# Performance work log

Hardware: AMD Instinct MI355X
Metric: run time of the kernel (lower is better)

Reference implementation:

```python
import jax, jax.numpy as jnp
import numpy as np

DEPTH = 10
WIDTH = 128
DIM = 2
N = 1_048_576


def setup_inputs() -> dict:
    key = jax.random.key(0)
    ks = jax.random.split(key, 14)
    x = jax.random.normal(ks[0], (N, DIM), jnp.float32)

    # Orthogonal init for the invertible 1x1 convs (QR of a random matrix),
    # matching Invertible1x1Conv.__init__.
    rng = np.random.default_rng(0)
    conv_w = np.stack([np.linalg.qr(rng.standard_normal((DIM, DIM)))[0]
                       for _ in range(DEPTH)]).astype(np.float32)

    def nrm(k, shape, sc=0.1):
        return sc * jax.random.normal(k, shape, jnp.float32)

    return dict(
        x=x,
        an_scale=jnp.exp(nrm(ks[1], (DEPTH, DIM))),          # outer actnorm, positive
        an_bias=nrm(ks[2], (DEPTH, DIM)),
        conv_w=jnp.asarray(conv_w),                           # [D, 2, 2]
        fc1_w=nrm(ks[3], (DEPTH, WIDTH, DIM // 2), 1.0),      # Linear(1, 128)
        fc1_b=nrm(ks[4], (DEPTH, WIDTH)),
        an1_scale=jnp.exp(nrm(ks[5], (DEPTH, WIDTH))),
        an1_bias=nrm(ks[6], (DEPTH, WIDTH)),
        fc2_w=nrm(ks[7], (DEPTH, WIDTH, WIDTH)),              # Linear(128, 128)
        fc2_b=nrm(ks[8], (DEPTH, WIDTH)),
        an2_scale=jnp.exp(nrm(ks[9], (DEPTH, WIDTH))),
        an2_bias=nrm(ks[10], (DEPTH, WIDTH)),
        fc3_w=nrm(ks[11], (DEPTH, DIM, WIDTH)),               # Linear(128, 2)
        fc3_b=nrm(ks[12], (DEPTH, DIM)),
        log_scale_factor=nrm(ks[13], (DEPTH, DIM)),
    )


def reference(x, an_scale, an_bias, conv_w, fc1_w, fc1_b, an1_scale, an1_bias,
              fc2_w, fc2_b, an2_scale, an2_bias, fc3_w, fc3_b, log_scale_factor):
    z = x
    logdet = jnp.zeros((x.shape[0],), x.dtype)
    half = DIM // 2
    for i in range(DEPTH):  # fixed depth=10, structurally distinct params
        # --- Actnorm ---
        z = (z - an_bias[i]) / an_scale[i]
        logdet = logdet - jnp.sum(jnp.log(jnp.abs(an_scale[i])))
        # --- Invertible 1x1 conv ---
        logdet = logdet + jnp.linalg.slogdet(conv_w[i])[1]
        z = z @ conv_w[i].T
        # --- Affine coupling (inner actnorms are already initialized) ---
        z_a, z_b = z[:, :half], z[:, half:]
        h = jax.nn.relu((z_b @ fc1_w[i].T + fc1_b[i] - an1_bias[i]) / an1_scale[i])
        h = jax.nn.relu((h @ fc2_w[i].T + fc2_b[i] - an2_bias[i]) / an2_scale[i])
        h = (h @ fc3_w[i].T + fc3_b[i]) * jnp.exp(log_scale_factor[i])  # [N, 2]
        t = h[:, 0::2]                         # [N, 1]
        s = jax.nn.sigmoid(h[:, 1::2] + 2.0)   # [N, 1]
        z = jnp.concatenate([s * z_a + t, z_b], axis=1)
        logdet = logdet + jnp.sum(jnp.log(s), axis=1)
    return z, logdet
```

## Files before the change

### kernel.cpp

```cpp
#include <hip/hip_runtime.h>
#include <math.h>


constexpr int kDepth = 10;
constexpr int kWidth = 128;
constexpr float kVMin = -24.0f;
constexpr float kVMax =  24.0f;

__global__ void prep_kernel(
    const float* __restrict__ an_scale, const float* __restrict__ an_bias,
    const float* __restrict__ conv_w,
    const float* __restrict__ fc1_w, const float* __restrict__ fc1_b,
    const float* __restrict__ an1_scale, const float* __restrict__ an1_bias,
    const float* __restrict__ fc2_w, const float* __restrict__ fc2_b,
    const float* __restrict__ an2_scale, const float* __restrict__ an2_bias,
    const float* __restrict__ fc3_b, const float* __restrict__ lsf,
    float* __restrict__ meta, float* __restrict__ kv,
    float* __restrict__ CG, float* __restrict__ CB)
{
  __shared__ float sWT[128 * 129];
  __shared__ float sVs[128], sG[128], sB[128];
  __shared__ float sGs[128], sBs[128];
  __shared__ int   sOrd[128];

  const int l = blockIdx.x;
  const int t = threadIdx.x;

  const float* wl = fc2_w + (size_t)l * kWidth * kWidth;
#pragma unroll 8
  for (int fi = t; fi < 128 * 128; fi += 256) {
    const int k = fi >> 7, j = fi & 127;
    sWT[j * 129 + k] = wl[fi];
  }

  if (t < 128) {
    const float s1 = an1_scale[l*kWidth + t];
    const float g = fc1_w[l*kWidth + t] / s1;
    const float b = (fc1_b[l*kWidth + t] - an1_bias[l*kWidth + t]) / s1;
    float vs, sg;
    if (g > 0.0f)      { vs = -b / g; sg =  1.0f; }
    else if (g < 0.0f) { vs = -b / g; sg = -1.0f; }
    else               { vs = (b > 0.0f) ? -1e30f : 1e30f; sg = (b > 0.0f) ? 1.0f : 0.0f; }
    sG[t] = g; sB[t] = b; sVs[t] = vs;
    sGs[t] = sg * g; sBs[t] = sg * b;
  }
  __syncthreads();

  if (t < 128) {
    const float my = sVs[t];
    int r = 0;
    const float4* vs4 = (const float4*)sVs;
#pragma unroll
    for (int i4 = 0; i4 < 32; ++i4) {
      float4 o = vs4[i4];
      const int ib = i4 * 4;
      r += (o.x < my) || (o.x == my && ib + 0 < t);
      r += (o.y < my) || (o.y == my && ib + 1 < t);
      r += (o.z < my) || (o.z == my && ib + 2 < t);
      r += (o.w < my) || (o.w == my && ib + 3 < t);
    }
    sOrd[r] = t;
  }
  __syncthreads();

  if (t < 128) {
    kv[l*128 + t] = sVs[sOrd[t]];

    float cg = 0.0f;
    float cb = fc2_b[l*kWidth + t] - an2_bias[l*kWidth + t];
    const float4* g4 = (const float4*)sG;
    const float4* b4 = (const float4*)sB;
#pragma unroll
    for (int j4 = 0; j4 < 32; ++j4) {
      float4 G = g4[j4], B = b4[j4];
      const int j = j4 * 4;
      float w0 = sWT[(j + 0) * 129 + t];
      float w1 = sWT[(j + 1) * 129 + t];
      float w2 = sWT[(j + 2) * 129 + t];
      float w3 = sWT[(j + 3) * 129 + t];
      if (G.x < 0.0f) { cg = fmaf(G.x, w0, cg); cb = fmaf(B.x, w0, cb); }
      if (G.y < 0.0f) { cg = fmaf(G.y, w1, cg); cb = fmaf(B.y, w1, cb); }
      if (G.z < 0.0f) { cg = fmaf(G.z, w2, cg); cb = fmaf(B.z, w2, cb); }
      if (G.w < 0.0f) { cg = fmaf(G.w, w3, cg); cb = fmaf(B.w, w3, cb); }
    }

    const size_t base = (size_t)l * 129 * 128;
    int4 J = ((const int4*)sOrd)[0];
    float w0 = sWT[J.x * 129 + t];
    float w1 = sWT[J.y * 129 + t];
    float w2 = sWT[J.z * 129 + t];
    float w3 = sWT[J.w * 129 + t];
#pragma unroll 1
    for (int c = 0; c < 32; ++c) {
      const int4 Jc = J;
      const float v0 = w0, v1 = w1, v2 = w2, v3 = w3;
      if (c + 1 < 32) {
        J = ((const int4*)sOrd)[c + 1];
        w0 = sWT[J.x * 129 + t];
        w1 = sWT[J.y * 129 + t];
        w2 = sWT[J.z * 129 + t];
        w3 = sWT[J.w * 129 + t];
      }
      const int p = c * 4;
      CG[base + (size_t)(p + 0) * 128 + t] = cg;
      CB[base + (size_t)(p + 0) * 128 + t] = cb;
      cg = fmaf(sGs[Jc.x], v0, cg); cb = fmaf(sBs[Jc.x], v0, cb);
      CG[base + (size_t)(p + 1) * 128 + t] = cg;
      CB[base + (size_t)(p + 1) * 128 + t] = cb;
      cg = fmaf(sGs[Jc.y], v1, cg); cb = fmaf(sBs[Jc.y], v1, cb);
      CG[base + (size_t)(p + 2) * 128 + t] = cg;
      CB[base + (size_t)(p + 2) * 128 + t] = cb;
      cg = fmaf(sGs[Jc.z], v2, cg); cb = fmaf(sBs[Jc.z], v2, cb);
      CG[base + (size_t)(p + 3) * 128 + t] = cg;
      CB[base + (size_t)(p + 3) * 128 + t] = cb;
      cg = fmaf(sGs[Jc.w], v3, cg); cb = fmaf(sBs[Jc.w], v3, cb);
    }
    CG[base + (size_t)128 * 128 + t] = cg;
    CB[base + (size_t)128 * 128 + t] = cb;
  }

  if (t == 0) {
    meta[16 + l*4 + 0] = expf(lsf[l*2 + 0]);
    meta[16 + l*4 + 1] = expf(lsf[l*2 + 1]);
    meta[16 + l*4 + 2] = fc3_b[l*2 + 0];
    meta[16 + l*4 + 3] = fc3_b[l*2 + 1];

    const float sx = an_scale[l*2+0], sy = an_scale[l*2+1];
    const float bx = an_bias[l*2+0],  by = an_bias[l*2+1];
    const float* cw = conv_w + l*4;
    const float m00 = cw[0]/sx, m01 = cw[1]/sy;
    const float m10 = cw[2]/sx, m11 = cw[3]/sy;
    meta[64 + l*8 + 0] = m00;
    meta[64 + l*8 + 1] = m01;
    meta[64 + l*8 + 2] = m10;
    meta[64 + l*8 + 3] = m11;
    meta[64 + l*8 + 4] = -(m00*bx + m01*by);
    meta[64 + l*8 + 5] = -(m10*bx + m11*by);
  }
  if (l == 0 && t == 0) {
    float cst = 0.0f;
    for (int i = 0; i < kDepth; ++i) {
      cst -= logf(fabsf(an_scale[i*2+0]));
      cst -= logf(fabsf(an_scale[i*2+1]));
      const float* cw = conv_w + i * 4;
      float det = cw[0]*cw[3] - cw[1]*cw[2];
      cst += logf(fabsf(det));
    }
    meta[0] = cst;
  }
}

__global__ __launch_bounds__(256) void table_kernel(
    const float* __restrict__ an2_scale,
    const float* __restrict__ fc3_w,
    const float* __restrict__ meta, const float* __restrict__ kv,
    const float* __restrict__ CG, const float* __restrict__ CB,
    int tabN, float4* __restrict__ tab)
{
  __shared__ float sKz[128], sKw[128], sKv[128];
  __shared__ int   sP[64];

  const int bpl   = tabN >> 6;
  const int l     = blockIdx.x / bpl;
  const int node0 = (blockIdx.x % bpl) * 64;
  const int t     = threadIdx.x;
  const float dv  = (kVMax - kVMin) / (float)(tabN - 1);

  if (t < 128) {
    const float si = 1.0f / an2_scale[l*kWidth + t];
    sKz[t] = fc3_w[l*2*kWidth + t] * si;
    sKw[t] = fc3_w[l*2*kWidth + kWidth + t] * si;
    sKv[t] = kv[l*128 + t];
  }
  __syncthreads();

  if (t < 64) {
    const float v = kVMin + dv * (float)(node0 + t);
    int p = 0;
    const float4* kv4 = (const float4*)sKv;
#pragma unroll
    for (int m = 0; m < 32; ++m) {
      float4 K = kv4[m];
      p += (K.x < v) + (K.y < v) + (K.z < v) + (K.w < v);
    }
    sP[t] = p;
  }
  __syncthreads();

  const int node = t >> 2, kq = t & 3;
  const int p = sP[node];
  const float v = kVMin + dv * (float)(node0 + node);

  const float4* cg4 = (const float4*)(CG + ((size_t)l*129 + p) * 128 + kq*32);
  const float4* cb4 = (const float4*)(CB + ((size_t)l*129 + p) * 128 + kq*32);
  const float4* kz4 = (const float4*)sKz + kq*8;
  const float4* kw4 = (const float4*)sKw + kq*8;

  float o0 = 0.f, o1 = 0.f, p0 = 0.f, p1 = 0.f;
#pragma unroll
  for (int c = 0; c < 8; ++c) {
    float4 G = cg4[c], B = cb4[c], Z = kz4[c], W = kw4[c];
    float raw, h, dd;
    raw = fmaf(v, G.x, B.x); h = fmaxf(raw, 0.f); dd = (raw > 0.f) ? G.x : 0.f;
    o0 = fmaf(h, Z.x, o0); o1 = fmaf(h, W.x, o1); p0 = fmaf(dd, Z.x, p0); p1 = fmaf(dd, W.x, p1);
    raw = fmaf(v, G.y, B.y); h = fmaxf(raw, 0.f); dd = (raw > 0.f) ? G.y : 0.f;
    o0 = fmaf(h, Z.y, o0); o1 = fmaf(h, W.y, o1); p0 = fmaf(dd, Z.y, p0); p1 = fmaf(dd, W.y, p1);
    raw = fmaf(v, G.z, B.z); h = fmaxf(raw, 0.f); dd = (raw > 0.f) ? G.z : 0.f;
    o0 = fmaf(h, Z.z, o0); o1 = fmaf(h, W.z, o1); p0 = fmaf(dd, Z.z, p0); p1 = fmaf(dd, W.z, p1);
    raw = fmaf(v, G.w, B.w); h = fmaxf(raw, 0.f); dd = (raw > 0.f) ? G.w : 0.f;
    o0 = fmaf(h, Z.w, o0); o1 = fmaf(h, W.w, o1); p0 = fmaf(dd, Z.w, p0); p1 = fmaf(dd, W.w, p1);
  }

  o0 += __shfl_xor(o0, 1); o0 += __shfl_xor(o0, 2);
  o1 += __shfl_xor(o1, 1); o1 += __shfl_xor(o1, 2);
  p0 += __shfl_xor(p0, 1); p0 += __shfl_xor(p0, 2);
  p1 += __shfl_xor(p1, 1); p1 += __shfl_xor(p1, 2);

  if (kq == 0) {
    const float E0  = meta[16 + l*4 + 0];
    const float E1  = meta[16 + l*4 + 1];
    const float b30 = meta[16 + l*4 + 2];
    const float b31 = meta[16 + l*4 + 3];
    tab[(size_t)l * tabN + node0 + node] =
        make_float4((o0 + b30) * E0, p0 * E0, (o1 + b31) * E1, p1 * E1);
  }
}

__device__ __forceinline__ unsigned int pack_bf16(float a, float b) {
  unsigned int ua = __float_as_uint(a);
  unsigned int ub = __float_as_uint(b);
  ua = (ua + 0x7FFFu + ((ua >> 16) & 1u)) >> 16;
  ub = (ub + 0x7FFFu + ((ub >> 16) & 1u)) >> 16;
  return ua | (ub << 16);
}

__global__ __launch_bounds__(1024) void flow_apply_kernel(
    const float* __restrict__ x,
    const float4* __restrict__ tab, const float* __restrict__ meta,
    int tabN,
    float* __restrict__ out_z, float* __restrict__ out_ld, int n)
{
  __shared__ float2       sTU[kDepth * 512];
  __shared__ unsigned int sPK[kDepth * 512];

  const int t = threadIdx.x;
  const int base = blockIdx.x * 2048;

  for (int j = t; j < kDepth * tabN; j += 1024) {
    float4 e = tab[j];
    sTU[j] = make_float2(e.x, e.z);
    sPK[j] = pack_bf16(e.y, e.w);
  }

  const int s0 = base + t;
  const int s1 = base + 1024 + t;
  const bool ok0 = s0 < n, ok1 = s1 < n;
  float2 z0 = ok0 ? reinterpret_cast<const float2*>(x)[s0] : make_float2(0.f, 0.f);
  float2 z1 = ok1 ? reinterpret_cast<const float2*>(x)[s1] : make_float2(0.f, 0.f);
  const float ldc = meta[0];
  float ld0 = ldc, ld1 = ldc;

  const float dv = (kVMax - kVMin) / (float)(tabN - 1);
  const float inv_dv = (float)(tabN - 1) / (kVMax - kVMin);
  const float offv = -kVMin * inv_dv;
  const float qmax = (float)(tabN - 1);
  constexpr float kLog2e = 1.44269504088896340736f;
  constexpr float kLn2   = 0.69314718055994530942f;

  __syncthreads();

#pragma unroll 1
  for (int i = 0; i < kDepth; ++i) {
    const float m00 = meta[64 + i*8 + 0], m01 = meta[64 + i*8 + 1];
    const float m10 = meta[64 + i*8 + 2], m11 = meta[64 + i*8 + 3];
    const float q0  = meta[64 + i*8 + 4], q1  = meta[64 + i*8 + 5];
    const float2* tu = sTU + i * tabN;
    const unsigned int* pk = sPK + i * tabN;

#pragma unroll
    for (int c = 0; c < 2; ++c) {
      float2& z  = c ? z1 : z0;
      float&  ld = c ? ld1 : ld0;
      const float na = fmaf(m00, z.x, fmaf(m01, z.y, q0));
      const float nb = fmaf(m10, z.x, fmaf(m11, z.y, q1));
      float xq = fmaf(nb, inv_dv, offv);
      xq = fminf(fmaxf(xq, 0.0f), qmax);
      const int qn = (int)(xq + 0.5f);
      const float2 e = tu[qn];
      const unsigned int d = pk[qn];
      const float dt = __uint_as_float(d << 16);
      const float du = __uint_as_float(d & 0xFFFF0000u);
      const float vn = fmaf((float)qn, dv, kVMin);
      const float f = nb - vn;
      const float tt = fmaf(f, dt, e.x);
      const float uu = fmaf(f, du, e.y);
      const float arg = uu + 2.0f;
      const float ev = __builtin_amdgcn_exp2f(arg * -kLog2e);
      const float den = 1.0f + ev;
      const float s = __builtin_amdgcn_rcpf(den);
      ld = fmaf(-kLn2, __builtin_amdgcn_logf(den), ld);
      z.x = fmaf(s, na, tt);
      z.y = nb;
    }
  }

  if (ok0) {
    reinterpret_cast<float2*>(out_z)[s0] = z0;
    out_ld[s0] = ld0;
  }
  if (ok1) {
    reinterpret_cast<float2*>(out_z)[s1] = z1;
    out_ld[s1] = ld1;
  }
}

extern "C" void kernel_launch(void* const* d_in, const int* in_sizes, int n_in,
                              void* d_out, int out_size, void* d_ws, size_t ws_size,
                              hipStream_t stream) {
  const float* x         = (const float*)d_in[0];
  const float* an_scale  = (const float*)d_in[1];
  const float* an_bias   = (const float*)d_in[2];
  const float* conv_w    = (const float*)d_in[3];
  const float* fc1_w     = (const float*)d_in[4];
  const float* fc1_b     = (const float*)d_in[5];
  const float* an1_scale = (const float*)d_in[6];
  const float* an1_bias  = (const float*)d_in[7];
  const float* fc2_w     = (const float*)d_in[8];
  const float* fc2_b     = (const float*)d_in[9];
  const float* an2_scale = (const float*)d_in[10];
  const float* an2_bias  = (const float*)d_in[11];
  const float* fc3_w     = (const float*)d_in[12];
  const float* fc3_b     = (const float*)d_in[13];
  const float* lsf       = (const float*)d_in[14];

  const int n = in_sizes[0] / 2;

  const size_t metaF = 256, kvF = (size_t)kDepth * 128;
  const size_t cF = (size_t)kDepth * 129 * 128;
  const size_t headF = metaF + kvF + 2 * cF;
  int tabN = 512;
  while (tabN > 128 &&
         headF * 4 + (size_t)kDepth * tabN * sizeof(float4) > ws_size) {
    tabN >>= 1;
  }
  float* meta = (float*)d_ws;
  float* kv   = meta + metaF;
  float* CG   = kv + kvF;
  float* CB   = CG + cF;
  float4* tab = (float4*)(CB + cF);

  prep_kernel<<<kDepth, 256, 0, stream>>>(
      an_scale, an_bias, conv_w, fc1_w, fc1_b, an1_scale, an1_bias,
      fc2_w, fc2_b, an2_scale, an2_bias, fc3_b, lsf,
      meta, kv, CG, CB);

  table_kernel<<<kDepth * (tabN / 64), 256, 0, stream>>>(
      an2_scale, fc3_w, meta, kv, CG, CB, tabN, tab);

  const int blocks = (n + 2047) / 2048;
  flow_apply_kernel<<<blocks, 1024, 0, stream>>>(
      x, tab, meta, tabN, (float*)d_out, (float*)d_out + (size_t)2 * n, n);
}
```

Baseline: 40.48 us.

## Split prefix-sum table build across four thread groups in prep kernel

The prep kernel now launches 512 threads per layer instead of 256. Each of four 128-thread groups computes its own starting prefix using ranks, then writes 32 of the 129 cumulative CG/CB rows. Before, a single group of 128 threads ran the whole 128-step serial chain. This shortens the serial critical path of a grid that has only 10 blocks, at the cost of a redundant 128-step initial reduction per group.

```diff
diff --git a/kernel.cpp b/kernel.cpp
--- a/kernel.cpp
+++ b/kernel.cpp
@@ -7,7 +7,7 @@
 constexpr float kVMin = -24.0f;
 constexpr float kVMax =  24.0f;
 
-__global__ void prep_kernel(
+__global__ __launch_bounds__(512) void prep_kernel(
     const float* __restrict__ an_scale, const float* __restrict__ an_bias,
     const float* __restrict__ conv_w,
     const float* __restrict__ fc1_w, const float* __restrict__ fc1_b,
@@ -21,14 +21,14 @@
   __shared__ float sWT[128 * 129];
   __shared__ float sVs[128], sG[128], sB[128];
   __shared__ float sGs[128], sBs[128];
-  __shared__ int   sOrd[128];
+  __shared__ int   sOrd[128], sRank[128];
 
   const int l = blockIdx.x;
   const int t = threadIdx.x;
-
   const float* wl = fc2_w + (size_t)l * kWidth * kWidth;
+
 #pragma unroll 8
-  for (int fi = t; fi < 128 * 128; fi += 256) {
+  for (int fi = t; fi < 128 * 128; fi += 512) {
     const int k = fi >> 7, j = fi & 127;
     sWT[j * 129 + k] = wl[fi];
   }
@@ -60,63 +60,63 @@
       r += (o.w < my) || (o.w == my && ib + 3 < t);
     }
     sOrd[r] = t;
-  }
-  __syncthreads();
-
-  if (t < 128) {
-    kv[l*128 + t] = sVs[sOrd[t]];
-
-    float cg = 0.0f;
-    float cb = fc2_b[l*kWidth + t] - an2_bias[l*kWidth + t];
-    const float4* g4 = (const float4*)sG;
-    const float4* b4 = (const float4*)sB;
-#pragma unroll
-    for (int j4 = 0; j4 < 32; ++j4) {
-      float4 G = g4[j4], B = b4[j4];
-      const int j = j4 * 4;
-      float w0 = sWT[(j + 0) * 129 + t];
-      float w1 = sWT[(j + 1) * 129 + t];
-      float w2 = sWT[(j + 2) * 129 + t];
-      float w3 = sWT[(j + 3) * 129 + t];
-      if (G.x < 0.0f) { cg = fmaf(G.x, w0, cg); cb = fmaf(B.x, w0, cb); }
-      if (G.y < 0.0f) { cg = fmaf(G.y, w1, cg); cb = fmaf(B.y, w1, cb); }
-      if (G.z < 0.0f) { cg = fmaf(G.z, w2, cg); cb = fmaf(B.z, w2, cb); }
-      if (G.w < 0.0f) { cg = fmaf(G.w, w3, cg); cb = fmaf(B.w, w3, cb); }
-    }
-
-    const size_t base = (size_t)l * 129 * 128;
-    int4 J = ((const int4*)sOrd)[0];
-    float w0 = sWT[J.x * 129 + t];
-    float w1 = sWT[J.y * 129 + t];
-    float w2 = sWT[J.z * 129 + t];
-    float w3 = sWT[J.w * 129 + t];
+    sRank[t] = r;
+  }
+  __syncthreads();
+
+  if (t < 128) kv[l*128 + t] = sVs[sOrd[t]];
+
+  const int g  = t >> 7;
+  const int k  = t & 127;
+  const int p0 = g * 32;
+
+  float cg = 0.0f;
+  float cb = fc2_b[l*kWidth + k] - an2_bias[l*kWidth + k];
+#pragma unroll 8
+  for (int j = 0; j < 128; ++j) {
+    const float w  = sWT[j * 129 + k];
+    const float gj = sG[j];
+    float ca = (gj < 0.0f) ? gj    : 0.0f;
+    float cc = (gj < 0.0f) ? sB[j] : 0.0f;
+    if (sRank[j] < p0) { ca += sGs[j]; cc += sBs[j]; }
+    cg = fmaf(ca, w, cg);
+    cb = fmaf(cc, w, cb);
+  }
+
+  const size_t base = (size_t)l * 129 * 128;
 #pragma unroll 1
-    for (int c = 0; c < 32; ++c) {
-      const int4 Jc = J;
-      const float v0 = w0, v1 = w1, v2 = w2, v3 = w3;
-      if (c + 1 < 32) {
-        J = ((const int4*)sOrd)[c + 1];
-        w0 = sWT[J.x * 129 + t];
-        w1 = sWT[J.y * 129 + t];
-        w2 = sWT[J.z * 129 + t];
-        w3 = sWT[J.w * 129 + t];
-      }
-      const int p = c * 4;
-      CG[base + (size_t)(p + 0) * 128 + t] = cg;
-      CB[base + (size_t)(p + 0) * 128 + t] = cb;
-      cg = fmaf(sGs[Jc.x], v0, cg); cb = fmaf(sBs[Jc.x], v0, cb);
-      CG[base + (size_t)(p + 1) * 128 + t] = cg;
-      CB[base + (size_t)(p + 1) * 128 + t] = cb;
-      cg = fmaf(sGs[Jc.y], v1, cg); cb = fmaf(sBs[Jc.y], v1, cb);
-      CG[base + (size_t)(p + 2) * 128 + t] = cg;
-      CB[base + (size_t)(p + 2) * 128 + t] = cb;
-      cg = fmaf(sGs[Jc.z], v2, cg); cb = fmaf(sBs[Jc.z], v2, cb);
-      CG[base + (size_t)(p + 3) * 128 + t] = cg;
-      CB[base + (size_t)(p + 3) * 128 + t] = cb;
-      cg = fmaf(sGs[Jc.w], v3, cg); cb = fmaf(sBs[Jc.w], v3, cb);
-    }
-    CG[base + (size_t)128 * 128 + t] = cg;
-    CB[base + (size_t)128 * 128 + t] = cb;
+  for (int c = 0; c < 4; ++c) {
+    const int pp = p0 + c * 8;
+    const int j0 = sOrd[pp + 0], j1 = sOrd[pp + 1];
+    const int j2 = sOrd[pp + 2], j3 = sOrd[pp + 3];
+    const int j4 = sOrd[pp + 4], j5 = sOrd[pp + 5];
+    const int j6 = sOrd[pp + 6], j7 = sOrd[pp + 7];
+    const float w0 = sWT[j0 * 129 + k], w1 = sWT[j1 * 129 + k];
+    const float w2 = sWT[j2 * 129 + k], w3 = sWT[j3 * 129 + k];
+    const float w4 = sWT[j4 * 129 + k], w5 = sWT[j5 * 129 + k];
+    const float w6 = sWT[j6 * 129 + k], w7 = sWT[j7 * 129 + k];
+    const float g0 = sGs[j0], b0 = sBs[j0];
+    const float g1 = sGs[j1], b1 = sBs[j1];
+    const float g2 = sGs[j2], b2 = sBs[j2];
+    const float g3 = sGs[j3], b3 = sBs[j3];
+    const float g4 = sGs[j4], b4 = sBs[j4];
+    const float g5 = sGs[j5], b5 = sBs[j5];
+    const float g6 = sGs[j6], b6 = sBs[j6];
+    const float g7 = sGs[j7], b7 = sBs[j7];
+    float* cgp = CG + base + (size_t)pp * 128 + k;
+    float* cbp = CB + base + (size_t)pp * 128 + k;
+    cgp[0*128] = cg; cbp[0*128] = cb; cg = fmaf(g0, w0, cg); cb = fmaf(b0, w0, cb);
+    cgp[1*128] = cg; cbp[1*128] = cb; cg = fmaf(g1, w1, cg); cb = fmaf(b1, w1, cb);
+    cgp[2*128] = cg; cbp[2*128] = cb; cg = fmaf(g2, w2, cg); cb = fmaf(b2, w2, cb);
+    cgp[3*128] = cg; cbp[3*128] = cb; cg = fmaf(g3, w3, cg); cb = fmaf(b3, w3, cb);
+    cgp[4*128] = cg; cbp[4*128] = cb; cg = fmaf(g4, w4, cg); cb = fmaf(b4, w4, cb);
+    cgp[5*128] = cg; cbp[5*128] = cb; cg = fmaf(g5, w5, cg); cb = fmaf(b5, w5, cb);
+    cgp[6*128] = cg; cbp[6*128] = cb; cg = fmaf(g6, w6, cg); cb = fmaf(b6, w6, cb);
+    cgp[7*128] = cg; cbp[7*128] = cb; cg = fmaf(g7, w7, cg); cb = fmaf(b7, w7, cb);
+  }
+  if (g == 3) {
+    CG[base + (size_t)128 * 128 + k] = cg;
+    CB[base + (size_t)128 * 128 + k] = cb;
   }
 
   if (t == 0) {
@@ -349,7 +349,7 @@
   float* CB   = CG + cF;
   float4* tab = (float4*)(CB + cF);
 
-  prep_kernel<<<kDepth, 256, 0, stream>>>(
+  prep_kernel<<<kDepth, 512, 0, stream>>>(
       an_scale, an_bias, conv_w, fc1_w, fc1_b, an1_scale, an1_bias,
       fc2_w, fc2_b, an2_scale, an2_bias, fc3_b, lsf,
       meta, kv, CG, CB);
```

Result: slower. 46.06 us (+13.8%).
